# Performance work log

Measured on AMD Instinct MI355X. Metric: run time of the kernel, lower is better.

The kernel has to match this reference:

```python
import jax, jax.numpy as jnp
import numpy as np

B, S, H, NH = 2, 2048, 1024, 16
HD = H // NH  # head dim = 64


def setup_inputs() -> dict:
    key = jax.random.key(0)
    ks = jax.random.split(key, 11)
    s = 1.0 / np.sqrt(H)
    return {
        "q": jax.random.normal(ks[0], (B, S, H), jnp.float32),
        "k": jax.random.normal(ks[1], (B, S, H), jnp.float32),
        "v": jax.random.normal(ks[2], (B, S, H), jnp.float32),
        "Wq": jax.random.normal(ks[3], (H, H), jnp.float32) * s,
        "bq": jax.random.normal(ks[4], (H,), jnp.float32) * 0.02,
        "Wk": jax.random.normal(ks[5], (H, H), jnp.float32) * s,
        "bk": jax.random.normal(ks[6], (H,), jnp.float32) * 0.02,
        "Wv": jax.random.normal(ks[7], (H, H), jnp.float32) * s,
        "bv": jax.random.normal(ks[8], (H,), jnp.float32) * 0.02,
        "Wo": jax.random.normal(ks[9], (H, H), jnp.float32) * s,
        "bo": jax.random.normal(ks[10], (H,), jnp.float32) * 0.02,
    }


def reference(q, k, v, Wq, bq, Wk, bk, Wv, bv, Wo, bo):
    # QKV projections: [B,S,H]
    qp = q @ Wq + bq
    kp = k @ Wk + bk
    vp = v @ Wv + bv
    # split heads -> [B, NH, S, HD]
    def split(x):
        return x.reshape(B, S, NH, HD).transpose(0, 2, 1, 3)
    qh, kh, vh = split(qp), split(kp), split(vp)
    # scores [B, NH, S, S], scale by sqrt(head_dim)
    scores = jnp.einsum('bhqd,bhkd->bhqk', qh, kh) / jnp.sqrt(jnp.asarray(HD, qh.dtype))
    attn = jax.nn.softmax(scores, axis=-1)  # attention_dropout p=0.0 (eval)
    ctx = jnp.einsum('bhqk,bhkd->bhqd', attn, vh)
    # merge heads -> [B, S, H]
    ctx = ctx.transpose(0, 2, 1, 3).reshape(B, S, H)
    out = ctx @ Wo + bo  # dropout p=0.0 (eval)
    return out
```

## Files before the change

### kernel.cpp

```cpp
#include <hip/hip_runtime.h>

typedef unsigned short u16;
typedef __attribute__((ext_vector_type(8))) short bf16x8;
typedef __attribute__((ext_vector_type(4))) float f32x4;
typedef __attribute__((ext_vector_type(16))) float f32x16;
typedef __attribute__((ext_vector_type(4))) unsigned short u16x4;
typedef __attribute__((ext_vector_type(4))) unsigned int u32x4;

#define B_  2
#define S_  2048
#define H_  1024
#define NH_ 16
#define HD_ 64
#define MR_ (B_*S_)
#define K_  H_

__device__ __forceinline__ u16 f2bf(float f) {
  union { float f; unsigned u; } x; x.f = f;
  unsigned r = x.u + 0x7fffu + ((x.u >> 16) & 1u);
  return (u16)(r >> 16);
}

__device__ __forceinline__ unsigned cvtpk(float lo, float hi) {
  unsigned r;
  asm("v_cvt_pk_bf16_f32 %0, %1, %2" : "=v"(r) : "v"(lo), "v"(hi));
  return r;
}

__device__ __forceinline__ void plswap(unsigned &a, unsigned &b) {
  asm("v_permlane32_swap_b32 %0, %1" : "+v"(a), "+v"(b));
}

__device__ __forceinline__ void gload16(const u16* g, u16* l) {
  __builtin_amdgcn_global_load_lds((const __attribute__((address_space(1))) void*)g,
                                   (__attribute__((address_space(3))) void*)l, 16, 0, 0);
}

__global__ __launch_bounds__(256) void prep(const float* __restrict__ q, const float* __restrict__ k,
                                            const float* __restrict__ v, const float* __restrict__ Wq,
                                            const float* __restrict__ Wk, const float* __restrict__ Wv,
                                            const float* __restrict__ Wo, u16* __restrict__ dst,
                                            u16* __restrict__ wt) {
  __shared__ float t[32][33];
  const int bid = blockIdx.x;
  if (bid < 12288) {
    const int z = bid >> 12;
    const float* src = z == 0 ? q : z == 1 ? k : v;
    u16* d = dst + (size_t)z * MR_ * H_;
    size_t i = ((size_t)(bid & 4095) * 256 + threadIdx.x) * 4;
    float4 f = *(const float4*)(src + i);
    u16x4 o = { f2bf(f.x), f2bf(f.y), f2bf(f.z), f2bf(f.w) };
    *(u16x4*)(d + i) = o;
  } else {
    const int r = bid - 12288;
    const int z = r >> 10;
    const float* W = z == 0 ? Wq : z == 1 ? Wk : z == 2 ? Wv : Wo;
    u16* Wt = wt + (size_t)z * H_ * K_;
    const int n0 = (r & 31) * 32, k0 = ((r >> 5) & 31) * 32;
    const int tx = threadIdx.x & 31, ty = threadIdx.x >> 5;
    #pragma unroll
    for (int i = 0; i < 4; i++) t[ty + 8*i][tx] = W[(size_t)(k0 + ty + 8*i) * H_ + n0 + tx];
    __syncthreads();
    #pragma unroll
    for (int i = 0; i < 4; i++) Wt[(size_t)(n0 + ty + 8*i) * K_ + k0 + tx] = f2bf(t[tx][ty + 8*i]);
  }
}

template <int MODE>
__device__ __forceinline__ void body256(const u16* __restrict__ A, const u16* __restrict__ Bt,
                                        const float* __restrict__ bias, float scale,
                                        u16* __restrict__ Obf, int mt, int nt,
                                        u16* lAbase, u16* lBbase) {
  const int tid = threadIdx.x;
  const int lane = tid & 63, wave = tid >> 6;
  const int wm = wave >> 2, wn = wave & 3;
  const int fr = lane & 15, kg = lane >> 4;
  const int m0 = mt * 256, n0 = nt * 256;

  const int srow = tid >> 3;
  const int sslot = (tid & 7) ^ (srow & 7);
  const u16* ga = A + (size_t)(m0 + srow) * K_ + sslot * 8;
  const u16* gb = Bt + (size_t)(n0 + srow) * K_ + sslot * 8;

  f32x4 acc[8][4] = {};

  #pragma unroll
  for (int j = 0; j < 4; j++) {
    gload16(ga + (size_t)(j * 64) * K_, lAbase + j * 4096 + tid * 8);
    gload16(gb + (size_t)(j * 64) * K_, lBbase + j * 4096 + tid * 8);
  }
  asm volatile("s_waitcnt vmcnt(0)" ::: "memory");
  __builtin_amdgcn_s_barrier();
  __builtin_amdgcn_sched_barrier(0);

  for (int s = 0; s < 16; ++s) {
    const int cur = s & 1;
    const u16* Acur = lAbase + cur * 16384;
    const u16* Bcur = lBbase + cur * 16384;
    u16* Anxt = lAbase + (cur ^ 1) * 16384;
    u16* Bnxt = lBbase + (cur ^ 1) * 16384;
    const size_t knext = (size_t)(s + 1) * 64;
    bf16x8 af[4][2];
    #pragma unroll
    for (int p = 0; p < 4; ++p) {
      const int mh = p >> 1, nh = p & 1;
      if ((p & 1) == 0) {
        #pragma unroll
        for (int mf2 = 0; mf2 < 4; ++mf2)
          #pragma unroll
          for (int kk = 0; kk < 2; ++kk)
            af[mf2][kk] = *(const bf16x8*)&Acur[(wm * 128 + mh * 64 + mf2 * 16 + fr) * 64 +
                                                ((((kk << 2) | kg) ^ (fr & 7)) << 3)];
      }
      bf16x8 bfr[2][2];
      #pragma unroll
      for (int nf2 = 0; nf2 < 2; ++nf2)
        #pragma unroll
        for (int kk = 0; kk < 2; ++kk)
          bfr[nf2][kk] = *(const bf16x8*)&Bcur[(wn * 64 + nh * 32 + nf2 * 16 + fr) * 64 +
                                               ((((kk << 2) | kg) ^ (fr & 7)) << 3)];
      if (s < 15 && p < 2) {
        #pragma unroll
        for (int jj = 0; jj < 2; ++jj) {
          const int j = p * 2 + jj;
          gload16(ga + (size_t)(j * 64) * K_ + knext, Anxt + j * 4096 + tid * 8);
          gload16(gb + (size_t)(j * 64) * K_ + knext, Bnxt + j * 4096 + tid * 8);
        }
      }
      __builtin_amdgcn_s_barrier();
      __builtin_amdgcn_s_setprio(1);
      #pragma unroll
      for (int mf2 = 0; mf2 < 4; ++mf2)
        #pragma unroll
        for (int nf2 = 0; nf2 < 2; ++nf2)
          #pragma unroll
          for (int kk = 0; kk < 2; ++kk)
            acc[mh * 4 + mf2][nh * 2 + nf2] = __builtin_amdgcn_mfma_f32_16x16x32_bf16(
                af[mf2][kk], bfr[nf2][kk], acc[mh * 4 + mf2][nh * 2 + nf2], 0, 0, 0);
      __builtin_amdgcn_s_setprio(0);
      if (p < 3) {
        __builtin_amdgcn_s_barrier();
      } else {
        asm volatile("s_waitcnt vmcnt(0)" ::: "memory");
        __builtin_amdgcn_s_barrier();
        __builtin_amdgcn_sched_barrier(0);
      }
    }
  }

  float bcol[4];
  #pragma unroll
  for (int nf = 0; nf < 4; nf++) bcol[nf] = bias[n0 + wn * 64 + nf * 16 + fr];

  if (MODE == 2) {
    #pragma unroll
    for (int mf = 0; mf < 8; mf++) {
      const int row0 = m0 + wm * 128 + mf * 16 + kg * 4;
      #pragma unroll
      for (int nf = 0; nf < 4; nf++) {
        const int col = n0 + wn * 64 + nf * 16 + fr;
        u16x4 o;
        #pragma unroll
        for (int r = 0; r < 4; r++) o[r] = f2bf(acc[mf][nf][r] + bcol[nf]);
        size_t idx = (((size_t)(col + ((row0 >> 11) << 10))) << 11) + (row0 & 2047);
        *(u16x4*)(Obf + idx) = o;
      }
    }
  } else {
    #pragma unroll
    for (int mf = 0; mf < 8; mf++)
      #pragma unroll
      for (int r = 0; r < 4; r++) {
        const int row = m0 + wm * 128 + mf * 16 + kg * 4 + r;
        #pragma unroll
        for (int nf = 0; nf < 4; nf++) {
          const int col = n0 + wn * 64 + nf * 16 + fr;
          Obf[(size_t)row * H_ + col] = f2bf((acc[mf][nf][r] + bcol[nf]) * scale);
        }
      }
  }
}

__global__ __launch_bounds__(512, 2) void gemm_qkv256(const u16* __restrict__ xb, const u16* __restrict__ wt,
                                                      const float* __restrict__ b0, const float* __restrict__ b1,
                                                      const float* __restrict__ b2,
                                                      u16* __restrict__ QKo, u16* __restrict__ VTo) {
  __shared__ u16 lA[2][256 * 64];
  __shared__ u16 lB[2][256 * 64];
  const int z = blockIdx.z;
  const int swz = (blockIdx.x << 3) + blockIdx.y;
  const int mt = swz >> 2, nt = swz & 3;
  const u16* A = xb + (size_t)z * MR_ * K_;
  const u16* Bt = wt + (size_t)z * H_ * K_;
  if (z == 2) {
    body256<2>(A, Bt, b2, 1.0f, VTo, mt, nt, &lA[0][0], &lB[0][0]);
  } else {
    const float* bias = z == 0 ? b0 : b1;
    const float scale = z == 0 ? 0.18033688011112042f : 1.0f;
    body256<0>(A, Bt, bias, scale, QKo + (size_t)z * MR_ * H_, mt, nt, &lA[0][0], &lB[0][0]);
  }
}

__device__ __forceinline__ void gemm_body_f32(const u16* __restrict__ A, const u16* __restrict__ Bt,
                                              const float* __restrict__ bias, float* __restrict__ Of,
                                              int m_tile, int n_tile) {
  __shared__ u16 ldsA[128 * 64];
  __shared__ u16 ldsB[128 * 64];
  const int tid = threadIdx.x;
  const int lane = tid & 63, wave = tid >> 6;
  const int wm = wave >> 1, wn = wave & 1;
  const int m0 = m_tile * 128, n0 = n_tile * 128;

  f32x4 acc[4][4] = {};

  const int srow = tid >> 3;
  const int sslot = (tid & 7) ^ (srow & 7);
  const u16* ga = A + (size_t)(m0 + srow) * K_ + sslot * 8;
  const u16* gb = Bt + (size_t)(n0 + srow) * K_ + sslot * 8;
  u16* la = ldsA + tid * 8;
  u16* lb = ldsB + tid * 8;

  const int fr = lane & 15;
  const int kg = lane >> 4;

  for (int k0 = 0; k0 < K_; k0 += 64) {
    #pragma unroll
    for (int j = 0; j < 4; j++) gload16(ga + (size_t)(j * 32) * K_ + k0, la + j * 2048);
    #pragma unroll
    for (int j = 0; j < 4; j++) gload16(gb + (size_t)(j * 32) * K_ + k0, lb + j * 2048);
    __syncthreads();

    #pragma unroll
    for (int kk = 0; kk < 2; kk++) {
      const int ps = (((kk << 2) | kg) ^ (fr & 7)) * 8;
      bf16x8 a[4], b[4];
      #pragma unroll
      for (int mf = 0; mf < 4; mf++)
        a[mf] = *(const bf16x8*)&ldsA[(wm * 64 + mf * 16 + fr) * 64 + ps];
      #pragma unroll
      for (int nf = 0; nf < 4; nf++)
        b[nf] = *(const bf16x8*)&ldsB[(wn * 64 + nf * 16 + fr) * 64 + ps];
      #pragma unroll
      for (int mf = 0; mf < 4; mf++)
        #pragma unroll
        for (int nf = 0; nf < 4; nf++)
          acc[mf][nf] = __builtin_amdgcn_mfma_f32_16x16x32_bf16(a[mf], b[nf], acc[mf][nf], 0, 0, 0);
    }
    __syncthreads();
  }

  float bcol[4];
  #pragma unroll
  for (int nf = 0; nf < 4; nf++) bcol[nf] = bias[n0 + wn * 64 + nf * 16 + fr];
  #pragma unroll
  for (int mf = 0; mf < 4; mf++)
    #pragma unroll
    for (int r = 0; r < 4; r++) {
      const int row = m0 + wm * 64 + mf * 16 + kg * 4 + r;
      #pragma unroll
      for (int nf = 0; nf < 4; nf++) {
        const int col = n0 + wn * 64 + nf * 16 + fr;
        Of[(size_t)row * H_ + col] = acc[mf][nf][r] + bcol[nf];
      }
    }
}

__global__ __launch_bounds__(256) void gemm_out(const u16* __restrict__ ctx, const u16* __restrict__ wot,
                                                const float* __restrict__ bo, float* __restrict__ out) {
  const int bid = blockIdx.x + (blockIdx.y << 3);
  const int swz = ((bid & 7) << 5) + (bid >> 3);
  gemm_body_f32(ctx, wot, bo, out, swz >> 3, swz & 7);
}

__global__ __launch_bounds__(512, 4) void attn(const u16* __restrict__ qp, const u16* __restrict__ kp,
                                               const u16* __restrict__ vt, u16* __restrict__ ctx) {
  __shared__ u16 Kl[2][2][64 * 64];
  __shared__ u16 Vl[2][2][64 * 64];
  __shared__ float mlbuf[2][4][32][2];
  const int bid = blockIdx.x + (blockIdx.y << 4);
  const int swz = ((bid & 7) << 6) + (bid >> 3);
  const int bh = swz >> 4;
  const int b = bh >> 4, h = bh & 15;
  const int q0 = (swz & 15) * 128;
  const int tid = threadIdx.x;
  const int g0 = tid >> 8;
  const int gt = tid & 255;
  const int w = (tid >> 6) & 3;
  const int l = tid & 63;
  const int ql = l & 31, hi = l >> 5;

  const u16* Q   = qp + (size_t)b * S_ * H_ + h * HD_;
  const u16* Kb  = kp + (size_t)b * S_ * H_ + h * HD_;
  const u16* Vtb = vt + (size_t)bh * HD_ * S_;
  u16* O = ctx + (size_t)b * S_ * H_ + h * HD_;

  const int srow = gt >> 3;
  const int sslot = (gt & 7) ^ (srow & 7);
  const int sbase = g0 << 10;

  const u16* Qrow = Q + (size_t)(q0 + w * 32 + ql) * H_;

  f32x16 oacc0 = {}, oacc1 = {};
  float m_run = -1e30f, l_run = 0.f;

  #pragma unroll
  for (int j = 0; j < 2; j++) {
    gload16(Kb + (size_t)(sbase + srow + 32 * j) * H_ + sslot * 8,
            &Kl[g0][0][0] + j * 2048 + gt * 8);
    gload16(Vtb + (size_t)(srow + 32 * j) * S_ + sbase + sslot * 8,
            &Vl[g0][0][0] + j * 2048 + gt * 8);
  }

  for (int it = 0; it < 16; ++it) {
    const int s0 = sbase + it * 64, cur = it & 1;
    __syncthreads();
    if (it + 1 < 16) {
      #pragma unroll
      for (int j = 0; j < 2; j++) {
        gload16(Kb + (size_t)(s0 + 64 + srow + 32 * j) * H_ + sslot * 8,
                &Kl[g0][cur ^ 1][0] + j * 2048 + gt * 8);
        gload16(Vtb + (size_t)(srow + 32 * j) * S_ + s0 + 64 + sslot * 8,
                &Vl[g0][cur ^ 1][0] + j * 2048 + gt * 8);
      }
    }
    f32x16 sc0 = {}, sc1 = {};
    __builtin_amdgcn_s_setprio(1);
    #pragma unroll
    for (int ds = 0; ds < 4; ds++) {
      const int sl = ((ds * 2 + hi) ^ (ql & 7)) << 3;
      bf16x8 qd = *(const bf16x8*)&Qrow[ds * 16 + hi * 8];
      bf16x8 k0 = *(const bf16x8*)&Kl[g0][cur][ql * 64 + sl];
      bf16x8 k1 = *(const bf16x8*)&Kl[g0][cur][(32 + ql) * 64 + sl];
      sc0 = __builtin_amdgcn_mfma_f32_32x32x16_bf16(k0, qd, sc0, 0, 0, 0);
      sc1 = __builtin_amdgcn_mfma_f32_32x32x16_bf16(k1, qd, sc1, 0, 0, 0);
    }
    __builtin_amdgcn_s_setprio(0);
    float t4[8];
    #pragma unroll
    for (int g = 0; g < 4; g++) {
      t4[g]     = fmaxf(fmaxf(sc0[4*g], sc0[4*g+1]), fmaxf(sc0[4*g+2], sc0[4*g+3]));
      t4[4 + g] = fmaxf(fmaxf(sc1[4*g], sc1[4*g+1]), fmaxf(sc1[4*g+2], sc1[4*g+3]));
    }
    float tmax = fmaxf(fmaxf(fmaxf(t4[0], t4[1]), fmaxf(t4[2], t4[3])),
                       fmaxf(fmaxf(t4[4], t4[5]), fmaxf(t4[6], t4[7])));
    tmax = fmaxf(tmax, __shfl_xor(tmax, 32, 64));
    if (!__all(tmax <= m_run + 8.0f)) {
      const float mn = fmaxf(m_run, tmax);
      const float sf = __builtin_amdgcn_exp2f(m_run - mn);
      m_run = mn;
      l_run *= sf;
      #pragma unroll
      for (int r = 0; r < 16; r++) {
        const float sfq = __shfl(sf, (r & 3) + 8 * (r >> 2) + 4 * hi, 64);
        oacc0[r] *= sfq;
        oacc1[r] *= sfq;
      }
    }
    float ps4[8];
    #pragma unroll
    for (int g = 0; g < 4; g++) {
      #pragma unroll
      for (int m = 0; m < 4; m++) {
        sc0[4*g+m] = __builtin_amdgcn_exp2f(sc0[4*g+m] - m_run);
        sc1[4*g+m] = __builtin_amdgcn_exp2f(sc1[4*g+m] - m_run);
      }
      ps4[g]     = (sc0[4*g] + sc0[4*g+1]) + (sc0[4*g+2] + sc0[4*g+3]);
      ps4[4 + g] = (sc1[4*g] + sc1[4*g+1]) + (sc1[4*g+2] + sc1[4*g+3]);
    }
    float psum = ((ps4[0] + ps4[1]) + (ps4[2] + ps4[3])) + ((ps4[4] + ps4[5]) + (ps4[6] + ps4[7]));
    psum += __shfl_xor(psum, 32, 64);
    l_run += psum;
    uint2 pk0[4], pk1[4];
    #pragma unroll
    for (int g = 0; g < 4; g++) {
      pk0[g].x = cvtpk(sc0[4*g], sc0[4*g+1]);  pk0[g].y = cvtpk(sc0[4*g+2], sc0[4*g+3]);
      pk1[g].x = cvtpk(sc1[4*g], sc1[4*g+1]);  pk1[g].y = cvtpk(sc1[4*g+2], sc1[4*g+3]);
    }
    __builtin_amdgcn_s_setprio(1);
    #pragma unroll
    for (int ks = 0; ks < 4; ks++) {
      const int ga = (ks & 1) * 2;
      unsigned x0, y0, x1, y1;
      if (ks < 2) { x0 = pk0[ga].x; y0 = pk0[ga].y; x1 = pk0[ga+1].x; y1 = pk0[ga+1].y; }
      else        { x0 = pk1[ga].x; y0 = pk1[ga].y; x1 = pk1[ga+1].x; y1 = pk1[ga+1].y; }
      plswap(x0, x1);
      plswap(y0, y1);
      u32x4 fu = { x0, y0, x1, y1 };
      const bf16x8 pfrag = __builtin_bit_cast(bf16x8, fu);
      #pragma unroll
      for (int dt = 0; dt < 2; dt++) {
        const int d = dt * 32 + ql;
        bf16x8 vf = *(const bf16x8*)&Vl[g0][cur][d * 64 + (((ks * 2 + hi) ^ (d & 7)) << 3)];
        if (dt == 0) oacc0 = __builtin_amdgcn_mfma_f32_32x32x16_bf16(pfrag, vf, oacc0, 0, 0, 0);
        else         oacc1 = __builtin_amdgcn_mfma_f32_32x32x16_bf16(pfrag, vf, oacc1, 0, 0, 0);
      }
    }
    __builtin_amdgcn_s_setprio(0);
  }

  if (l < 32) { mlbuf[g0][w][ql][0] = m_run; mlbuf[g0][w][ql][1] = l_run; }
  __syncthreads();
  const float m_o = mlbuf[g0 ^ 1][w][ql][0];
  const float l_o = mlbuf[g0 ^ 1][w][ql][1];
  const float m_tot = fmaxf(m_run, m_o);
  const float a_s = __builtin_amdgcn_exp2f(m_run - m_tot);
  const float rinv = 1.0f / (l_run * a_s + l_o * __builtin_amdgcn_exp2f(m_o - m_tot));
  float ar[16], rr[16];
  #pragma unroll
  for (int r = 0; r < 16; r++) {
    const int qi = (r & 3) + 8 * (r >> 2) + 4 * hi;
    ar[r] = __shfl(a_s, qi, 64);
    rr[r] = __shfl(rinv, qi, 64);
  }

  float* cb = (float*)(&Kl[0][0][0]);
  float* cw = cb + w * 2048 + l;
  if (g0 == 1) {
    #pragma unroll
    for (int r = 0; r < 16; r++) {
      cw[r * 64]        = oacc0[r] * ar[r];
      cw[(16 + r) * 64] = oacc1[r] * ar[r];
    }
  }
  __syncthreads();
  if (g0 == 0) {
    #pragma unroll
    for (int r = 0; r < 16; r++) {
      const int qi = (r & 3) + 8 * (r >> 2) + 4 * hi;
      const int row = q0 + w * 32 + qi;
      O[(size_t)row * H_ + ql]      = f2bf((oacc0[r] * ar[r] + cw[r * 64]) * rr[r]);
      O[(size_t)row * H_ + 32 + ql] = f2bf((oacc1[r] * ar[r] + cw[(16 + r) * 64]) * rr[r]);
    }
  }
}

extern "C" void kernel_launch(void* const* d_in, const int* in_sizes, int n_in,
                              void* d_out, int out_size, void* d_ws, size_t ws_size,
                              hipStream_t stream) {
  const float* q  = (const float*)d_in[0];
  const float* k  = (const float*)d_in[1];
  const float* v  = (const float*)d_in[2];
  const float* Wq = (const float*)d_in[3];
  const float* bq = (const float*)d_in[4];
  const float* Wk = (const float*)d_in[5];
  const float* bk = (const float*)d_in[6];
  const float* Wv = (const float*)d_in[7];
  const float* bv = (const float*)d_in[8];
  const float* Wo = (const float*)d_in[9];
  const float* bo = (const float*)d_in[10];
  float* out = (float*)d_out;

  char* ws = (char*)d_ws;
  const size_t MB = 1024 * 1024;
  u16* xb   = (u16*)(ws);
  u16* wt   = (u16*)(ws + 24 * MB);
  u16* qkp  = (u16*)(ws + 32 * MB);
  u16* vtp  = (u16*)(ws + 48 * MB);
  u16* ctx  = (u16*)(ws);

  prep      <<<dim3(16384),     256, 0, stream>>>(q, k, v, Wq, Wk, Wv, Wo, xb, wt);
  gemm_qkv256<<<dim3(8, 8, 3),  512, 0, stream>>>(xb, wt, bq, bk, bv, qkp, vtp);
  attn      <<<dim3(16, 32),    512, 0, stream>>>(qkp, qkp + (size_t)MR_ * H_, vtp, ctx);
  gemm_out  <<<dim3(8, 32, 1),  256, 0, stream>>>(ctx, wt + (size_t)3 * H_ * K_, bo, out);
}
```

Baseline: 131.3 us.

## Fuse fp32-to-bf16 activation conversion into QKV GEMM A-tile loads

Removes the separate prep pass that converted q/k/v to bf16 in workspace. The QKV GEMM now reads fp32 activations into registers, converts them with v_cvt_pk_bf16_f32 and writes them to LDS, prefetching the next k-slice. This saves a full write and re-read of the bf16 activations. In exchange the GEMM reads twice the A bytes per tile, and the register-staged path replaces async global_load_lds, which adds register pressure and VALU work inside the main loop.

```diff
diff --git a/kernel.cpp b/kernel.cpp
--- a/kernel.cpp
+++ b/kernel.cpp
@@ -36,38 +36,26 @@
                                    (__attribute__((address_space(3))) void*)l, 16, 0, 0);
 }
 
-__global__ __launch_bounds__(256) void prep(const float* __restrict__ q, const float* __restrict__ k,
-                                            const float* __restrict__ v, const float* __restrict__ Wq,
-                                            const float* __restrict__ Wk, const float* __restrict__ Wv,
-                                            const float* __restrict__ Wo, u16* __restrict__ dst,
+__global__ __launch_bounds__(256) void prep(const float* __restrict__ Wq, const float* __restrict__ Wk,
+                                            const float* __restrict__ Wv, const float* __restrict__ Wo,
                                             u16* __restrict__ wt) {
   __shared__ float t[32][33];
   const int bid = blockIdx.x;
-  if (bid < 12288) {
-    const int z = bid >> 12;
-    const float* src = z == 0 ? q : z == 1 ? k : v;
-    u16* d = dst + (size_t)z * MR_ * H_;
-    size_t i = ((size_t)(bid & 4095) * 256 + threadIdx.x) * 4;
-    float4 f = *(const float4*)(src + i);
-    u16x4 o = { f2bf(f.x), f2bf(f.y), f2bf(f.z), f2bf(f.w) };
-    *(u16x4*)(d + i) = o;
-  } else {
-    const int r = bid - 12288;
-    const int z = r >> 10;
-    const float* W = z == 0 ? Wq : z == 1 ? Wk : z == 2 ? Wv : Wo;
-    u16* Wt = wt + (size_t)z * H_ * K_;
-    const int n0 = (r & 31) * 32, k0 = ((r >> 5) & 31) * 32;
-    const int tx = threadIdx.x & 31, ty = threadIdx.x >> 5;
-    #pragma unroll
-    for (int i = 0; i < 4; i++) t[ty + 8*i][tx] = W[(size_t)(k0 + ty + 8*i) * H_ + n0 + tx];
-    __syncthreads();
-    #pragma unroll
-    for (int i = 0; i < 4; i++) Wt[(size_t)(n0 + ty + 8*i) * K_ + k0 + tx] = f2bf(t[tx][ty + 8*i]);
-  }
+  const int z = bid >> 10;
+  const int r = bid & 1023;
+  const float* W = z == 0 ? Wq : z == 1 ? Wk : z == 2 ? Wv : Wo;
+  u16* Wt = wt + (size_t)z * H_ * K_;
+  const int n0 = (r & 31) * 32, k0 = (r >> 5) * 32;
+  const int tx = threadIdx.x & 31, ty = threadIdx.x >> 5;
+  #pragma unroll
+  for (int i = 0; i < 4; i++) t[ty + 8*i][tx] = W[(size_t)(k0 + ty + 8*i) * H_ + n0 + tx];
+  __syncthreads();
+  #pragma unroll
+  for (int i = 0; i < 4; i++) Wt[(size_t)(n0 + ty + 8*i) * K_ + k0 + tx] = f2bf(t[tx][ty + 8*i]);
 }
 
 template <int MODE>
-__device__ __forceinline__ void body256(const u16* __restrict__ A, const u16* __restrict__ Bt,
+__device__ __forceinline__ void body256(const float* __restrict__ Af, const u16* __restrict__ Bt,
                                         const float* __restrict__ bias, float scale,
                                         u16* __restrict__ Obf, int mt, int nt,
                                         u16* lAbase, u16* lBbase) {
@@ -79,17 +67,28 @@
 
   const int srow = tid >> 3;
   const int sslot = (tid & 7) ^ (srow & 7);
-  const u16* ga = A + (size_t)(m0 + srow) * K_ + sslot * 8;
+  const float* gaf = Af + (size_t)(m0 + srow) * K_ + sslot * 8;
   const u16* gb = Bt + (size_t)(n0 + srow) * K_ + sslot * 8;
 
   f32x4 acc[8][4] = {};
 
-  #pragma unroll
-  for (int j = 0; j < 4; j++) {
-    gload16(ga + (size_t)(j * 64) * K_, lAbase + j * 4096 + tid * 8);
-    gload16(gb + (size_t)(j * 64) * K_, lBbase + j * 4096 + tid * 8);
-  }
-  asm volatile("s_waitcnt vmcnt(0)" ::: "memory");
+  {
+    float4 lo[4], hi[4];
+    #pragma unroll
+    for (int j = 0; j < 4; j++) {
+      const float* p = gaf + (size_t)(j * 64) * K_;
+      lo[j] = *(const float4*)p;
+      hi[j] = *(const float4*)(p + 4);
+      gload16(gb + (size_t)(j * 64) * K_, lBbase + j * 4096 + tid * 8);
+    }
+    #pragma unroll
+    for (int j = 0; j < 4; j++) {
+      u32x4 wv = { cvtpk(lo[j].x, lo[j].y), cvtpk(lo[j].z, lo[j].w),
+                   cvtpk(hi[j].x, hi[j].y), cvtpk(hi[j].z, hi[j].w) };
+      *(u32x4*)(lAbase + j * 4096 + tid * 8) = wv;
+    }
+  }
+  asm volatile("s_waitcnt vmcnt(0) lgkmcnt(0)" ::: "memory");
   __builtin_amdgcn_s_barrier();
   __builtin_amdgcn_sched_barrier(0);
 
@@ -100,6 +99,17 @@
     u16* Anxt = lAbase + (cur ^ 1) * 16384;
     u16* Bnxt = lBbase + (cur ^ 1) * 16384;
     const size_t knext = (size_t)(s + 1) * 64;
+
+    float4 alo[4], ahi[4];
+    if (s < 15) {
+      #pragma unroll
+      for (int j = 0; j < 4; j++) {
+        const float* p = gaf + (size_t)(j * 64) * K_ + knext;
+        alo[j] = *(const float4*)p;
+        ahi[j] = *(const float4*)(p + 4);
+      }
+    }
+
     bf16x8 af[4][2];
     #pragma unroll
     for (int p = 0; p < 4; ++p) {
@@ -123,8 +133,16 @@
         #pragma unroll
         for (int jj = 0; jj < 2; ++jj) {
           const int j = p * 2 + jj;
-          gload16(ga + (size_t)(j * 64) * K_ + knext, Anxt + j * 4096 + tid * 8);
           gload16(gb + (size_t)(j * 64) * K_ + knext, Bnxt + j * 4096 + tid * 8);
+        }
+      }
+      if (s < 15 && p >= 2) {
+        #pragma unroll
+        for (int jj = 0; jj < 2; ++jj) {
+          const int j = (p - 2) * 2 + jj;
+          u32x4 wv = { cvtpk(alo[j].x, alo[j].y), cvtpk(alo[j].z, alo[j].w),
+                       cvtpk(ahi[j].x, ahi[j].y), cvtpk(ahi[j].z, ahi[j].w) };
+          *(u32x4*)(Anxt + j * 4096 + tid * 8) = wv;
         }
       }
       __builtin_amdgcn_s_barrier();
@@ -141,7 +159,7 @@
       if (p < 3) {
         __builtin_amdgcn_s_barrier();
       } else {
-        asm volatile("s_waitcnt vmcnt(0)" ::: "memory");
+        asm volatile("s_waitcnt vmcnt(0) lgkmcnt(0)" ::: "memory");
         __builtin_amdgcn_s_barrier();
         __builtin_amdgcn_sched_barrier(0);
       }
@@ -181,7 +199,8 @@
   }
 }
 
-__global__ __launch_bounds__(512, 2) void gemm_qkv256(const u16* __restrict__ xb, const u16* __restrict__ wt,
+__global__ __launch_bounds__(512, 2) void gemm_qkv256(const float* __restrict__ q, const float* __restrict__ k,
+                                                      const float* __restrict__ v, const u16* __restrict__ wt,
                                                       const float* __restrict__ b0, const float* __restrict__ b1,
                                                       const float* __restrict__ b2,
                                                       u16* __restrict__ QKo, u16* __restrict__ VTo) {
@@ -190,7 +209,7 @@
   const int z = blockIdx.z;
   const int swz = (blockIdx.x << 3) + blockIdx.y;
   const int mt = swz >> 2, nt = swz & 3;
-  const u16* A = xb + (size_t)z * MR_ * K_;
+  const float* A = z == 0 ? q : z == 1 ? k : v;
   const u16* Bt = wt + (size_t)z * H_ * K_;
   if (z == 2) {
     body256<2>(A, Bt, b2, 1.0f, VTo, mt, nt, &lA[0][0], &lB[0][0]);
@@ -452,14 +471,13 @@
 
   char* ws = (char*)d_ws;
   const size_t MB = 1024 * 1024;
-  u16* xb   = (u16*)(ws);
+  u16* ctx  = (u16*)(ws);
   u16* wt   = (u16*)(ws + 24 * MB);
   u16* qkp  = (u16*)(ws + 32 * MB);
   u16* vtp  = (u16*)(ws + 48 * MB);
-  u16* ctx  = (u16*)(ws);
-
-  prep      <<<dim3(16384),     256, 0, stream>>>(q, k, v, Wq, Wk, Wv, Wo, xb, wt);
-  gemm_qkv256<<<dim3(8, 8, 3),  512, 0, stream>>>(xb, wt, bq, bk, bv, qkp, vtp);
+
+  prep      <<<dim3(4096),      256, 0, stream>>>(Wq, Wk, Wv, Wo, wt);
+  gemm_qkv256<<<dim3(8, 8, 3),  512, 0, stream>>>(q, k, v, wt, bq, bk, bv, qkp, vtp);
   attn      <<<dim3(16, 32),    512, 0, stream>>>(qkp, qkp + (size_t)MR_ * H_, vtp, ctx);
   gemm_out  <<<dim3(8, 32, 1),  256, 0, stream>>>(ctx, wt + (size_t)3 * H_ * K_, bo, out);
 }
```

Measured after the change: 131.4 us. About the same (+0.1%).
